# Performance work log

Measured on AMD Instinct MI355X. Metric: run time of the kernel, lower is better.

Reference implementation:

```python
import jax, jax.numpy as jnp
import numpy as np

H = W = 192
C = 256
MAX_FEATURES = 2048
NUM_UP = 4  # num_upsampling scaling steps: pos -> pos*2 + 0.5 each step

# HandcraftedLocalizationModule filters (D2-Net)
DI  = [[0., -0.5, 0.], [0., 0., 0.], [0., 0.5, 0.]]
DJ  = [[0., 0., 0.], [-0.5, 0., 0.5], [0., 0., 0.]]
DII = [[0., 1., 0.], [0., -2., 0.], [0., 1., 0.]]
DJJ = [[0., 0., 0.], [1., -2., 1.], [0., 0., 0.]]
DIJ = [[0.25, 0., -0.25], [0., 0., 0.], [-0.25, 0., 0.25]]


def _conv3(x, k):
    # x: [H,W]; 3x3 cross-correlation, padding 1 (matches F.conv2d)
    k = jnp.asarray(k, x.dtype)
    return jax.lax.conv_general_dilated(x[None, None], k[None, None],
                                        window_strides=(1, 1),
                                        padding=[(1, 1), (1, 1)])[0, 0]


def _process_scale(feat, score):
    # feat: [C,H,W] dense descriptors, score: [H,W] attention/detection map
    Hm, Wm = score.shape
    # --- NMS: 3x3 maxpool, keep only local maxima (x[lmax != x] = 0) ---
    lmax = jax.lax.reduce_window(score, -jnp.inf, jax.lax.max,
                                 (3, 3), (1, 1), [(1, 1), (1, 1)])
    det = jnp.where(lmax == score, score, 0.0)
    valid = det != 0.0  # torch.nonzero equivalent (fixed-shape mask)
    # --- handcrafted localization (2x2 Newton step on the raw score map) ---
    di, dj = _conv3(score, DI), _conv3(score, DJ)
    dii, djj, dij = _conv3(score, DII), _conv3(score, DJJ), _conv3(score, DIJ)
    dd = dii * djj - dij * dij
    dd = jnp.where(dd == 0.0, 1e-20, dd)  # degenerate Hessian -> huge step, rejected by |.|<0.5
    step_i = -(djj * di - dij * dj) / dd
    step_j = -(-dij * di + dii * dj) / dd
    valid &= (jnp.abs(step_i) < 0.5) & (jnp.abs(step_j) < 0.5)
    ii, jj = jnp.meshgrid(jnp.arange(Hm, dtype=score.dtype),
                          jnp.arange(Wm, dtype=score.dtype), indexing='ij')
    ki = jnp.where(valid, ii + step_i, 0.0)
    kj = jnp.where(valid, jj + step_j, 0.0)
    # --- bilinear interpolation of dense features at sub-pixel keypoints ---
    i0 = jnp.floor(ki)
    j0 = jnp.floor(kj)
    valid &= (i0 >= 0) & (j0 >= 0) & (i0 + 1 <= Hm - 1) & (j0 + 1 <= Wm - 1)
    i0c = jnp.clip(i0, 0, Hm - 2).astype(jnp.int32)
    j0c = jnp.clip(j0, 0, Wm - 2).astype(jnp.int32)
    wi = ki - i0c
    wj = kj - j0c
    desc = (feat[:, i0c, j0c] * (1 - wi) * (1 - wj)
            + feat[:, i0c, j0c + 1] * (1 - wi) * wj
            + feat[:, i0c + 1, j0c] * wi * (1 - wj)
            + feat[:, i0c + 1, j0c + 1] * wi * wj)  # [C,H,W]
    norm = jnp.maximum(jnp.sqrt(jnp.sum(desc * desc, axis=0)), 1e-12)
    desc = desc / norm  # F.normalize(dim=0)
    # --- upscale positions: pos = pos*2 + 0.5 repeated NUM_UP times ---
    for _ in range(NUM_UP):
        ki = ki * 2 + 0.5
        kj = kj * 2 + 0.5
    scores = jnp.where(valid, det, -jnp.inf)  # invalid padded with -inf
    kp = jnp.stack([kj, ki], axis=-1).reshape(-1, 2)  # [:, [1,0]] swap -> (x, y)
    return kp, desc.reshape(desc.shape[0], -1).T, scores.reshape(-1), det


def setup_inputs() -> dict:
    key = jax.random.key(0)
    ks = jax.random.split(key, 6)
    return {
        "feat_early": jax.random.normal(ks[0], (1, C, H, W), jnp.float32),
        "feat_middle": jax.random.normal(ks[1], (1, C, H, W), jnp.float32),
        "feat_deep": jax.random.normal(ks[2], (1, C, H, W), jnp.float32),
        "score_early": jax.random.uniform(ks[3], (1, 1, H, W), jnp.float32),
        "score_middle": jax.random.uniform(ks[4], (1, 1, H, W), jnp.float32),
        "score_deep": jax.random.uniform(ks[5], (1, 1, H, W), jnp.float32),
    }


def reference(feat_early, feat_middle, feat_deep, score_early, score_middle, score_deep):
    feats = [feat_early[0], feat_middle[0], feat_deep[0]]
    smaps = [score_early[0, 0], score_middle[0, 0], score_deep[0, 0]]
    kps, descs, scs, dets = zip(*[_process_scale(f, s) for f, s in zip(feats, smaps)])
    kp = jnp.concatenate(kps)      # [3HW, 2]
    desc = jnp.concatenate(descs)  # [3HW, C]
    sc = jnp.concatenate(scs)      # [3HW]
    # torch.sort(descending) + thresh/max_features cap == top_k over padded scores
    top_s, idx = jax.lax.top_k(sc, MAX_FEATURES)
    sel = jnp.isfinite(top_s)
    keypoints = jnp.where(sel[:, None], kp[idx], 0.0)
    descriptors = jnp.where(sel[:, None], desc[idx], 0.0)
    scores = jnp.where(sel, top_s, 0.0)
    return keypoints, descriptors, scores, dets[0], dets[1], dets[2]
```

## Files before the change

kernel.cpp:

```cpp
#include <hip/hip_runtime.h>

#pragma clang fp contract(off)

#define H_ 192
#define W_ 192
#define HW_ (192 * 192)
#define NSC 3
#define NCAND (NSC * HW_)
#define CCH 256
#define KMAX 2048
#define NBIN 4096

#define KP_OFF 0
#define DESC_OFF (KMAX * 2)
#define SC_OFF (DESC_OFF + KMAX * CCH)
#define DET_OFF (SC_OFF + KMAX)

typedef unsigned long long u64;
typedef unsigned int u32;

#define CNT_OFF 884736
#define SLOT_OFF 884800
#define GH_OFF 917568
#define SARR_OFF 933952
#define CUR_OFF 950400
#define SURV_OFF 966784

__device__ __forceinline__ u32 key_bin(u32 sb) {
    if (sb >= 0xBF800000u) return NBIN - 1;
    if (sb >= 0xBF000000u) return 2048u + ((sb >> 12) & 0x7FFu);
    return (sb >> 20) & 0x7FFu;
}

__device__ __forceinline__ void newton_pixel(const float* __restrict__ sm, int i, int j,
                                             float& det, float& ki, float& kj, bool& valid) {
    float v[3][3];
#pragma unroll
    for (int a = 0; a < 3; ++a) {
#pragma unroll
        for (int b = 0; b < 3; ++b) {
            int ii = i + a - 1, jj = j + b - 1;
            bool in = (ii >= 0) && (ii < H_) && (jj >= 0) && (jj < W_);
            v[a][b] = in ? sm[ii * W_ + jj] : 0.0f;
        }
    }
    float c = v[1][1];
    float mx = v[0][0];
    mx = fmaxf(mx, v[0][1]); mx = fmaxf(mx, v[0][2]);
    mx = fmaxf(mx, v[1][0]); mx = fmaxf(mx, c);
    mx = fmaxf(mx, v[1][2]); mx = fmaxf(mx, v[2][0]);
    mx = fmaxf(mx, v[2][1]); mx = fmaxf(mx, v[2][2]);
    det = (mx == c) ? c : 0.0f;
    float di  = -0.5f * v[0][1] + 0.5f * v[2][1];
    float dj  = -0.5f * v[1][0] + 0.5f * v[1][2];
    float dii = v[0][1] - 2.0f * c + v[2][1];
    float djj = v[1][0] - 2.0f * c + v[1][2];
    float dij = 0.25f * v[0][0] - 0.25f * v[0][2] - 0.25f * v[2][0] + 0.25f * v[2][2];
    float dd = dii * djj - dij * dij;
    if (dd == 0.0f) dd = 1e-20f;
    float step_i = -(djj * di - dij * dj) / dd;
    float step_j = -(-dij * di + dii * dj) / dd;
    valid = (det != 0.0f) && (fabsf(step_i) < 0.5f) && (fabsf(step_j) < 0.5f);
    ki = valid ? ((float)i + step_i) : 0.0f;
    kj = valid ? ((float)j + step_j) : 0.0f;
    float i0 = floorf(ki), j0 = floorf(kj);
    valid = valid && (i0 >= 0.0f) && (j0 >= 0.0f) &&
            (i0 + 1.0f <= (float)(H_ - 1)) && (j0 + 1.0f <= (float)(W_ - 1));
}

__device__ __forceinline__ void decode_gid(u32 gid, int& s, int& i, int& j) {
    s = (int)(gid / HW_);
    int rem = (int)gid - s * HW_;
    i = rem / W_;
    j = rem - i * W_;
}

__global__ __launch_bounds__(256) void cand_kernel(
    const float* __restrict__ s0, const float* __restrict__ s1, const float* __restrict__ s2,
    float* __restrict__ out, u64* __restrict__ fin, u32* __restrict__ cnts,
    u32* __restrict__ ghist) {
    __shared__ u32 lcnt, base;
    int tid = threadIdx.x;
    if (tid == 0) lcnt = 0;
    __syncthreads();
    int t = blockIdx.x * 256 + tid;
    bool valid = false;
    u64 key = 0;
    {
        int s, i, j;
        decode_gid((u32)t, s, i, j);
        const float* sm = (s == 0) ? s0 : (s == 1) ? s1 : s2;
        float det, ki, kj;
        newton_pixel(sm, i, j, det, ki, kj, valid);
        out[DET_OFF + t] = det;
        if (valid) {
            u32 sb = __float_as_uint(det) | 0x80000000u;
            key = ((u64)sb << 32) | (u64)(0xFFFFFFFFu - (u32)t);
            atomicAdd(&ghist[key_bin(sb)], 1u);
        }
    }
    u32 lpos = 0;
    if (valid) lpos = atomicAdd(&lcnt, 1u);
    __syncthreads();
    if (tid == 0 && lcnt > 0) base = atomicAdd(&cnts[0], lcnt);
    __syncthreads();
    if (valid) fin[base + lpos] = key;
}

__global__ __launch_bounds__(256) void scan_kernel(
    const u32* __restrict__ ghist, u32* __restrict__ sarr, u32* __restrict__ cursor,
    u32* __restrict__ cnts) {
    __shared__ u32 ls[NBIN + 1];
    __shared__ u32 lT[256];
    int t = threadIdx.x;
    u32 chunk[16];
    u32 acc = 0;
#pragma unroll
    for (int k = 15; k >= 0; --k) {
        acc += ghist[t * 16 + k];
        chunk[k] = acc;
    }
    lT[t] = acc;
    __syncthreads();
    for (int off = 1; off < 256; off <<= 1) {
        u32 v = lT[t] + ((t + off < 256) ? lT[t + off] : 0u);
        __syncthreads();
        lT[t] = v;
        __syncthreads();
    }
    u32 add = (t < 255) ? lT[t + 1] : 0u;
#pragma unroll
    for (int k = 0; k < 16; ++k) ls[t * 16 + k] = chunk[k] + add;
    if (t == 0) ls[NBIN] = 0;
    __syncthreads();
#pragma unroll
    for (int k = 0; k < 16; ++k) {
        u32 b = t * 16 + k;
        sarr[b] = ls[b];
        cursor[b] = ls[b + 1];
        if (ls[b + 1] < KMAX && (b == 0 || ls[b] >= KMAX)) cnts[2] = ls[b];
    }
    if (t == 0) sarr[NBIN] = 0;
}

__global__ __launch_bounds__(256) void scatter_kernel(
    const u64* __restrict__ fin, const u32* __restrict__ sarr, u32* __restrict__ cursor,
    u32* __restrict__ cnts, u64* __restrict__ surv) {
    u32 n = cnts[0];
    for (u32 idx = blockIdx.x * 256 + threadIdx.x; idx < n; idx += 64 * 256) {
        u64 key = fin[idx];
        u32 b = key_bin((u32)(key >> 32));
        if (sarr[b + 1] < KMAX) {
            u32 pos = atomicAdd(&cursor[b], 1u);
            surv[pos] = key;
        }
    }
}

__global__ __launch_bounds__(256) void rank_kernel(
    const u64* __restrict__ surv, const u32* __restrict__ sarr, const u32* __restrict__ cnts,
    const float* __restrict__ s0, const float* __restrict__ s1, const float* __restrict__ s2,
    float4* __restrict__ slot) {
    u32 m = cnts[2];
    for (u32 p = blockIdx.x * 256 + threadIdx.x; p < m; p += 32 * 256) {
        u64 key = surv[p];
        u32 b = key_bin((u32)(key >> 32));
        u32 lo = sarr[b + 1], hi = sarr[b];
        u32 rank = lo;
        for (u32 q = lo; q < hi; ++q) rank += (surv[q] > key) ? 1u : 0u;
        if (rank < KMAX) {
            u32 gid = 0xFFFFFFFFu - (u32)(key & 0xFFFFFFFFull);
            int s, i, j;
            decode_gid(gid, s, i, j);
            const float* sm = (s == 0) ? s0 : (s == 1) ? s1 : s2;
            float det, ki, kj;
            bool valid;
            newton_pixel(sm, i, j, det, ki, kj, valid);
            slot[rank] = make_float4(ki, kj, det, (float)s);
        }
    }
}

__global__ __launch_bounds__(256) void output_kernel(
    const float4* __restrict__ slot,
    const float* __restrict__ f0, const float* __restrict__ f1, const float* __restrict__ f2,
    float* __restrict__ out) {
    int lane = threadIdx.x & 63;
    int r = blockIdx.x * 4 + (threadIdx.x >> 6);
    float4 info = slot[r];
    bool pad = (info.z == 0.0f);
    float ki = info.x, kj = info.y;
    int s = (int)info.w;
    const float* feat = (s == 0) ? f0 : (s == 1) ? f1 : f2;
    int i0 = (int)floorf(ki), j0 = (int)floorf(kj);
    float wi = ki - (float)i0;
    float wj = kj - (float)j0;
    const float* p = feat + (size_t)lane * HW_ + i0 * W_ + j0;
    float d[4];
    float sq = 0.0f;
#pragma unroll
    for (int k = 0; k < 4; ++k) {
        const float* q = p + (size_t)k * 64 * HW_;
        float f00 = q[0], f01 = q[1], f10 = q[W_], f11 = q[W_ + 1];
        d[k] = f00 * (1.0f - wi) * (1.0f - wj) + f01 * (1.0f - wi) * wj +
               f10 * wi * (1.0f - wj) + f11 * wi * wj;
        sq += d[k] * d[k];
    }
#pragma unroll
    for (int o = 1; o < 64; o <<= 1) sq += __shfl_xor(sq, o, 64);
    float norm = fmaxf(sqrtf(sq), 1e-12f);
#pragma unroll
    for (int k = 0; k < 4; ++k)
        out[DESC_OFF + r * CCH + k * 64 + lane] = pad ? 0.0f : d[k] / norm;
    if (lane == 0) {
        float x = kj, y = ki;
#pragma unroll
        for (int u = 0; u < 4; ++u) { x = x * 2.0f + 0.5f; y = y * 2.0f + 0.5f; }
        out[SC_OFF + r] = pad ? 0.0f : info.z;
        out[KP_OFF + r * 2 + 0] = pad ? 0.0f : x;
        out[KP_OFF + r * 2 + 1] = pad ? 0.0f : y;
    }
}

extern "C" void kernel_launch(void* const* d_in, const int* in_sizes, int n_in,
                              void* d_out, int out_size, void* d_ws, size_t ws_size,
                              hipStream_t stream) {
    const float* f0 = (const float*)d_in[0];
    const float* f1 = (const float*)d_in[1];
    const float* f2 = (const float*)d_in[2];
    const float* s0 = (const float*)d_in[3];
    const float* s1 = (const float*)d_in[4];
    const float* s2 = (const float*)d_in[5];
    float* out = (float*)d_out;

    char* ws = (char*)d_ws;
    u64* fin = (u64*)ws;
    u32* cnts = (u32*)(ws + CNT_OFF);
    float4* slot = (float4*)(ws + SLOT_OFF);
    u32* ghist = (u32*)(ws + GH_OFF);
    u32* sarr = (u32*)(ws + SARR_OFF);
    u32* cursor = (u32*)(ws + CUR_OFF);
    u64* surv = (u64*)(ws + SURV_OFF);

    hipMemsetAsync(ws + CNT_OFF, 0, 64 + KMAX * 16 + NBIN * 4, stream);
    cand_kernel<<<NCAND / 256, 256, 0, stream>>>(s0, s1, s2, out, fin, cnts, ghist);
    scan_kernel<<<1, 256, 0, stream>>>(ghist, sarr, cursor, cnts);
    scatter_kernel<<<64, 256, 0, stream>>>(fin, sarr, cursor, cnts, surv);
    rank_kernel<<<32, 256, 0, stream>>>(surv, sarr, cnts, s0, s1, s2, slot);
    output_kernel<<<KMAX / 4, 256, 0, stream>>>(slot, f0, f1, f2, out);
}
```

Measured before the change: 165.4 us.

## Fold scan and rank kernels into scatter and output via per-block LDS suffix scan

Removes the single-block scan kernel and the rank kernel. Each scatter and output block now recomputes the 4096-bin suffix scan of the histogram in LDS. The output kernel binary-searches the bin holding its rank, ranks that bin's survivors cooperatively within a wavefront, then recomputes the Newton step and does the bilinear gather directly. This cuts two launches and a global slot round-trip, at the cost of redundant histogram scans in every block and per-wave rank loops over each bin's contents.

```diff
diff --git a/kernel.cpp b/kernel.cpp
--- a/kernel.cpp
+++ b/kernel.cpp
@@ -20,11 +20,10 @@
 typedef unsigned int u32;
 
 #define CNT_OFF 884736
-#define SLOT_OFF 884800
-#define GH_OFF 917568
-#define SARR_OFF 933952
-#define CUR_OFF 950400
-#define SURV_OFF 966784
+#define GH_OFF 884800
+#define CUR_OFF 901184
+#define SURV_OFF 917568
+#define ZERO_BYTES 32832
 
 __device__ __forceinline__ u32 key_bin(u32 sb) {
     if (sb >= 0xBF800000u) return NBIN - 1;
@@ -75,6 +74,31 @@
     j = rem - i * W_;
 }
 
+__device__ __forceinline__ void lds_suffix_scan(const u32* __restrict__ ghist,
+                                                u32* ls, u32* lT) {
+    int t = threadIdx.x;
+    u32 chunk[16];
+    u32 acc = 0;
+#pragma unroll
+    for (int k = 15; k >= 0; --k) {
+        acc += ghist[t * 16 + k];
+        chunk[k] = acc;
+    }
+    lT[t] = acc;
+    __syncthreads();
+    for (int off = 1; off < 256; off <<= 1) {
+        u32 v = lT[t] + ((t + off < 256) ? lT[t + off] : 0u);
+        __syncthreads();
+        lT[t] = v;
+        __syncthreads();
+    }
+    u32 add = (t < 255) ? lT[t + 1] : 0u;
+#pragma unroll
+    for (int k = 0; k < 16; ++k) ls[t * 16 + k] = chunk[k] + add;
+    if (t == 0) ls[NBIN] = 0;
+    __syncthreads();
+}
+
 __global__ __launch_bounds__(256) void cand_kernel(
     const float* __restrict__ s0, const float* __restrict__ s1, const float* __restrict__ s2,
     float* __restrict__ out, u64* __restrict__ fin, u32* __restrict__ cnts,
@@ -107,90 +131,74 @@
     if (valid) fin[base + lpos] = key;
 }
 
-__global__ __launch_bounds__(256) void scan_kernel(
-    const u32* __restrict__ ghist, u32* __restrict__ sarr, u32* __restrict__ cursor,
-    u32* __restrict__ cnts) {
+__global__ __launch_bounds__(256) void scatter_kernel(
+    const u64* __restrict__ fin, const u32* __restrict__ ghist, u32* __restrict__ cursor,
+    const u32* __restrict__ cnts, u64* __restrict__ surv) {
     __shared__ u32 ls[NBIN + 1];
     __shared__ u32 lT[256];
-    int t = threadIdx.x;
-    u32 chunk[16];
-    u32 acc = 0;
-#pragma unroll
-    for (int k = 15; k >= 0; --k) {
-        acc += ghist[t * 16 + k];
-        chunk[k] = acc;
-    }
-    lT[t] = acc;
-    __syncthreads();
-    for (int off = 1; off < 256; off <<= 1) {
-        u32 v = lT[t] + ((t + off < 256) ? lT[t + off] : 0u);
-        __syncthreads();
-        lT[t] = v;
-        __syncthreads();
-    }
-    u32 add = (t < 255) ? lT[t + 1] : 0u;
-#pragma unroll
-    for (int k = 0; k < 16; ++k) ls[t * 16 + k] = chunk[k] + add;
-    if (t == 0) ls[NBIN] = 0;
-    __syncthreads();
-#pragma unroll
-    for (int k = 0; k < 16; ++k) {
-        u32 b = t * 16 + k;
-        sarr[b] = ls[b];
-        cursor[b] = ls[b + 1];
-        if (ls[b + 1] < KMAX && (b == 0 || ls[b] >= KMAX)) cnts[2] = ls[b];
-    }
-    if (t == 0) sarr[NBIN] = 0;
-}
-
-__global__ __launch_bounds__(256) void scatter_kernel(
-    const u64* __restrict__ fin, const u32* __restrict__ sarr, u32* __restrict__ cursor,
-    u32* __restrict__ cnts, u64* __restrict__ surv) {
+    lds_suffix_scan(ghist, ls, lT);
     u32 n = cnts[0];
     for (u32 idx = blockIdx.x * 256 + threadIdx.x; idx < n; idx += 64 * 256) {
         u64 key = fin[idx];
         u32 b = key_bin((u32)(key >> 32));
-        if (sarr[b + 1] < KMAX) {
-            u32 pos = atomicAdd(&cursor[b], 1u);
-            surv[pos] = key;
-        }
-    }
-}
-
-__global__ __launch_bounds__(256) void rank_kernel(
-    const u64* __restrict__ surv, const u32* __restrict__ sarr, const u32* __restrict__ cnts,
+        u32 seglo = ls[b + 1];
+        if (seglo < KMAX) {
+            u32 off = atomicAdd(&cursor[b], 1u);
+            surv[seglo + off] = key;
+        }
+    }
+}
+
+__global__ __launch_bounds__(256) void output_kernel(
+    const u64* __restrict__ surv, const u32* __restrict__ ghist,
     const float* __restrict__ s0, const float* __restrict__ s1, const float* __restrict__ s2,
-    float4* __restrict__ slot) {
-    u32 m = cnts[2];
-    for (u32 p = blockIdx.x * 256 + threadIdx.x; p < m; p += 32 * 256) {
-        u64 key = surv[p];
-        u32 b = key_bin((u32)(key >> 32));
-        u32 lo = sarr[b + 1], hi = sarr[b];
-        u32 rank = lo;
-        for (u32 q = lo; q < hi; ++q) rank += (surv[q] > key) ? 1u : 0u;
-        if (rank < KMAX) {
-            u32 gid = 0xFFFFFFFFu - (u32)(key & 0xFFFFFFFFull);
-            int s, i, j;
-            decode_gid(gid, s, i, j);
-            const float* sm = (s == 0) ? s0 : (s == 1) ? s1 : s2;
-            float det, ki, kj;
-            bool valid;
-            newton_pixel(sm, i, j, det, ki, kj, valid);
-            slot[rank] = make_float4(ki, kj, det, (float)s);
-        }
-    }
-}
-
-__global__ __launch_bounds__(256) void output_kernel(
-    const float4* __restrict__ slot,
     const float* __restrict__ f0, const float* __restrict__ f1, const float* __restrict__ f2,
     float* __restrict__ out) {
-    int lane = threadIdx.x & 63;
-    int r = blockIdx.x * 4 + (threadIdx.x >> 6);
-    float4 info = slot[r];
-    bool pad = (info.z == 0.0f);
-    float ki = info.x, kj = info.y;
-    int s = (int)info.w;
+    __shared__ u32 ls[NBIN + 1];
+    __shared__ u32 lT[256];
+    lds_suffix_scan(ghist, ls, lT);
+    int tid = threadIdx.x;
+    int lane = tid & 63;
+    int r = blockIdx.x * 4 + (tid >> 6);
+    u32 n = ls[0];
+    u32 nwin = (n < KMAX) ? n : KMAX;
+    if ((u32)r >= nwin) {
+#pragma unroll
+        for (int k = 0; k < 4; ++k) out[DESC_OFF + r * CCH + k * 64 + lane] = 0.0f;
+        if (lane == 0) {
+            out[SC_OFF + r] = 0.0f;
+            out[KP_OFF + r * 2 + 0] = 0.0f;
+            out[KP_OFF + r * 2 + 1] = 0.0f;
+        }
+        return;
+    }
+    u32 blo = 0, bhi = NBIN;
+    while (bhi - blo > 1) {
+        u32 mid = (blo + bhi) >> 1;
+        if (ls[mid] > (u32)r) blo = mid; else bhi = mid;
+    }
+    u32 b = blo;
+    u32 seglo = ls[b + 1], seghi = ls[b];
+    u64 mykey = 0;
+    bool mine = false;
+    for (u32 p = seglo + (u32)lane; p < seghi; p += 64) {
+        u64 key = surv[p];
+        u32 rk = seglo;
+        for (u32 q = seglo; q < seghi; ++q) rk += (surv[q] > key) ? 1u : 0u;
+        if (rk == (u32)r) { mykey = key; mine = true; }
+    }
+    u64 bal = __ballot(mine);
+    int src = __ffsll((unsigned long long)bal) - 1;
+    u32 klo = (u32)__shfl((int)(u32)(mykey & 0xFFFFFFFFull), src, 64);
+    u32 khi = (u32)__shfl((int)(u32)(mykey >> 32), src, 64);
+    u64 key = ((u64)khi << 32) | (u64)klo;
+    u32 gid = 0xFFFFFFFFu - (u32)(key & 0xFFFFFFFFull);
+    int s, i, j;
+    decode_gid(gid, s, i, j);
+    const float* sm = (s == 0) ? s0 : (s == 1) ? s1 : s2;
+    float det, ki, kj;
+    bool valid;
+    newton_pixel(sm, i, j, det, ki, kj, valid);
     const float* feat = (s == 0) ? f0 : (s == 1) ? f1 : f2;
     int i0 = (int)floorf(ki), j0 = (int)floorf(kj);
     float wi = ki - (float)i0;
@@ -211,14 +219,14 @@
     float norm = fmaxf(sqrtf(sq), 1e-12f);
 #pragma unroll
     for (int k = 0; k < 4; ++k)
-        out[DESC_OFF + r * CCH + k * 64 + lane] = pad ? 0.0f : d[k] / norm;
+        out[DESC_OFF + r * CCH + k * 64 + lane] = d[k] / norm;
     if (lane == 0) {
         float x = kj, y = ki;
 #pragma unroll
         for (int u = 0; u < 4; ++u) { x = x * 2.0f + 0.5f; y = y * 2.0f + 0.5f; }
-        out[SC_OFF + r] = pad ? 0.0f : info.z;
-        out[KP_OFF + r * 2 + 0] = pad ? 0.0f : x;
-        out[KP_OFF + r * 2 + 1] = pad ? 0.0f : y;
+        out[SC_OFF + r] = det;
+        out[KP_OFF + r * 2 + 0] = x;
+        out[KP_OFF + r * 2 + 1] = y;
     }
 }
 
@@ -236,16 +244,12 @@
     char* ws = (char*)d_ws;
     u64* fin = (u64*)ws;
     u32* cnts = (u32*)(ws + CNT_OFF);
-    float4* slot = (float4*)(ws + SLOT_OFF);
     u32* ghist = (u32*)(ws + GH_OFF);
-    u32* sarr = (u32*)(ws + SARR_OFF);
     u32* cursor = (u32*)(ws + CUR_OFF);
     u64* surv = (u64*)(ws + SURV_OFF);
 
-    hipMemsetAsync(ws + CNT_OFF, 0, 64 + KMAX * 16 + NBIN * 4, stream);
+    hipMemsetAsync(ws + CNT_OFF, 0, ZERO_BYTES, stream);
     cand_kernel<<<NCAND / 256, 256, 0, stream>>>(s0, s1, s2, out, fin, cnts, ghist);
-    scan_kernel<<<1, 256, 0, stream>>>(ghist, sarr, cursor, cnts);
-    scatter_kernel<<<64, 256, 0, stream>>>(fin, sarr, cursor, cnts, surv);
-    rank_kernel<<<32, 256, 0, stream>>>(surv, sarr, cnts, s0, s1, s2, slot);
-    output_kernel<<<KMAX / 4, 256, 0, stream>>>(slot, f0, f1, f2, out);
-}
+    scatter_kernel<<<64, 256, 0, stream>>>(fin, ghist, cursor, cnts, surv);
+    output_kernel<<<KMAX / 4, 256, 0, stream>>>(surv, ghist, s0, s1, s2, f0, f1, f2, out);
+}
```

Result: faster. 156.8 us (median of 2 runs) (-5.2%).
